# Optimization experiments

Measured on AMD Instinct MI355X. Metric: run time of the kernel, lower is better.

The kernel has to match this reference:

```python
import jax, jax.numpy as jnp
import numpy as np

N = 50000      # nodes
E = 1600000    # edges (avg degree 32)
F_IN = 3       # PROTEINS num_node_features
H = 64         # dim_h
G = 512        # num graphs in batch
C = 2          # PROTEINS num_classes
BN_EPS = 1e-5


def setup_inputs() -> dict:
    key = jax.random.key(0)
    ks = iter(jax.random.split(key, 64))

    def rn(shape, s=0.1):
        return (jax.random.normal(next(ks), shape) * s).astype(jnp.float32)

    inp = {"x": rn((N, F_IN), 1.0)}
    for li, din in ((1, F_IN), (2, H), (3, H)):
        p = f"conv{li}_"
        inp[p + "w1"] = rn((din, H))
        inp[p + "b1"] = rn((H,))
        inp[p + "bn_g"] = jnp.ones((H,), jnp.float32)
        inp[p + "bn_b"] = jnp.zeros((H,), jnp.float32)
        inp[p + "bn_m"] = rn((H,))
        inp[p + "bn_v"] = jax.random.uniform(next(ks), (H,), jnp.float32, 0.5, 1.5)
        inp[p + "w2"] = rn((H, H))
        inp[p + "b2"] = rn((H,))
    inp["lin1_w"] = rn((3 * H, 3 * H))
    inp["lin1_b"] = rn((3 * H,))
    inp["lin2_w"] = rn((3 * H, C))
    inp["lin2_b"] = rn((C,))
    inp["edge_index"] = jax.random.randint(next(ks), (2, E), 0, N, jnp.int64)
    inp["batch"] = jnp.sort(jax.random.randint(next(ks), (N,), 0, G, jnp.int64))
    return inp


def gin_conv(x, src, dst, w1, b1, g, bb, m, v, w2, b2):
    # GINConv, eps=0: mlp(x + sum_{j->i} x_j); aggregate messages at target (dst)
    agg = jax.ops.segment_sum(x[src], dst, num_segments=N)  # [N, d]
    h = x + agg
    h = h @ w1 + b1
    h = (h - m) * jax.lax.rsqrt(v + BN_EPS) * g + bb  # BatchNorm1d (eval)
    h = jax.nn.relu(h)
    h = jax.nn.relu(h @ w2 + b2)
    return h


def reference(x,
              conv1_w1, conv1_b1, conv1_bn_g, conv1_bn_b, conv1_bn_m, conv1_bn_v, conv1_w2, conv1_b2,
              conv2_w1, conv2_b1, conv2_bn_g, conv2_bn_b, conv2_bn_m, conv2_bn_v, conv2_w2, conv2_b2,
              conv3_w1, conv3_b1, conv3_bn_g, conv3_bn_b, conv3_bn_m, conv3_bn_v, conv3_w2, conv3_b2,
              lin1_w, lin1_b, lin2_w, lin2_b,
              edge_index, batch):
    src, dst = edge_index[0], edge_index[1]
    h1 = gin_conv(x,  src, dst, conv1_w1, conv1_b1, conv1_bn_g, conv1_bn_b, conv1_bn_m, conv1_bn_v, conv1_w2, conv1_b2)
    h2 = gin_conv(h1, src, dst, conv2_w1, conv2_b1, conv2_bn_g, conv2_bn_b, conv2_bn_m, conv2_bn_v, conv2_w2, conv2_b2)
    h3 = gin_conv(h2, src, dst, conv3_w1, conv3_b1, conv3_bn_g, conv3_bn_b, conv3_bn_m, conv3_bn_v, conv3_w2, conv3_b2)
    # global_add_pool per graph
    p1 = jax.ops.segment_sum(h1, batch, num_segments=G)
    p2 = jax.ops.segment_sum(h2, batch, num_segments=G)
    p3 = jax.ops.segment_sum(h3, batch, num_segments=G)
    h = jnp.concatenate((p1, p2, p3), axis=1)          # [G, 3H]
    h = jax.nn.relu(h @ lin1_w + lin1_b)
    # dropout p=0.5 is identity in eval mode
    h = h @ lin2_w + lin2_b                            # [G, C]
    return (h, jax.nn.log_softmax(h, axis=1))
```

## Files before the change

### kernel.cpp

```cpp
#include <hip/hip_runtime.h>
#include <hip/hip_bf16.h>
#include <math.h>

#define N_NODES 50000
#define N_EDGES 1600000
#define H 64
#define G_GRAPHS 512
#define C_CLS 2
#define BN_EPS 1e-5f
#define NBUCK 196
#define BUCKCAP 16384
#define E4 (N_EDGES / 4)
#define CSR_BLOCKS ((E4 + 511) / 512)
#define IOP 72

typedef __attribute__((ext_vector_type(8))) short short8;
typedef __attribute__((ext_vector_type(4))) float floatx4;

__device__ __forceinline__ float bflo(unsigned int u) { return __uint_as_float(u << 16); }
__device__ __forceinline__ float bfhi(unsigned int u) { return __uint_as_float(u & 0xffff0000u); }
__device__ __forceinline__ unsigned int bf16_rne(float f) {
    unsigned int u = __float_as_uint(f);
    u += 0x7fffu + ((u >> 16) & 1u);
    return u >> 16;
}

__global__ __launch_bounds__(256) void prep_kernel(
    const float* __restrict__ w2_0, const float* __restrict__ w1_1,
    const float* __restrict__ w2_1, const float* __restrict__ w1_2,
    const float* __restrict__ w2_2, unsigned short* __restrict__ wt,
    const float* __restrict__ x, uint2* __restrict__ xb) {
    int b = blockIdx.x, t = threadIdx.x;
    if (b < 5) {
        const float* w = (b == 0) ? w2_0 : (b == 1) ? w1_1 : (b == 2) ? w2_1
                         : (b == 3) ? w1_2 : w2_2;
        unsigned short* o = wt + b * (H * H);
        for (int idx = t; idx < H * H; idx += 256) {
            int k = idx >> 6, j = idx & 63;
            o[j * H + k] = (unsigned short)bf16_rne(w[idx]);
        }
    } else {
        int node = (b - 5) * 256 + t;
        if (node < N_NODES) {
            uint2 p;
            p.x = bf16_rne(x[node * 3 + 0]) | (bf16_rne(x[node * 3 + 1]) << 16);
            p.y = bf16_rne(x[node * 3 + 2]);
            xb[node] = p;
        }
    }
}

__global__ __launch_bounds__(256) void scatter1_kernel(const int* __restrict__ src,
                                                       const int* __restrict__ dst,
                                                       int* __restrict__ gcnt,
                                                       int* __restrict__ gpacked) {
    __shared__ int bh[NBUCK];
    int t = threadIdx.x;
    if (t < NBUCK) bh[t] = 0;
    __syncthreads();
    int base = blockIdx.x * 512;

    int pkA[4], bkA[4], lrA[4]; bool vA = false;
    int pkB[4], bkB[4], lrB[4]; bool vB = false;
    {
        int i = base + t;
        if (i < E4) {
            vA = true;
            int4 s4 = ((const int4*)src)[i];
            int4 d4 = ((const int4*)dst)[i];
            bkA[0] = d4.x >> 8; pkA[0] = ((d4.x & 255) << 16) | s4.x; lrA[0] = atomicAdd(&bh[bkA[0]], 1);
            bkA[1] = d4.y >> 8; pkA[1] = ((d4.y & 255) << 16) | s4.y; lrA[1] = atomicAdd(&bh[bkA[1]], 1);
            bkA[2] = d4.z >> 8; pkA[2] = ((d4.z & 255) << 16) | s4.z; lrA[2] = atomicAdd(&bh[bkA[2]], 1);
            bkA[3] = d4.w >> 8; pkA[3] = ((d4.w & 255) << 16) | s4.w; lrA[3] = atomicAdd(&bh[bkA[3]], 1);
        }
    }
    {
        int i = base + 256 + t;
        if (i < E4) {
            vB = true;
            int4 s4 = ((const int4*)src)[i];
            int4 d4 = ((const int4*)dst)[i];
            bkB[0] = d4.x >> 8; pkB[0] = ((d4.x & 255) << 16) | s4.x; lrB[0] = atomicAdd(&bh[bkB[0]], 1);
            bkB[1] = d4.y >> 8; pkB[1] = ((d4.y & 255) << 16) | s4.y; lrB[1] = atomicAdd(&bh[bkB[1]], 1);
            bkB[2] = d4.z >> 8; pkB[2] = ((d4.z & 255) << 16) | s4.z; lrB[2] = atomicAdd(&bh[bkB[2]], 1);
            bkB[3] = d4.w >> 8; pkB[3] = ((d4.w & 255) << 16) | s4.w; lrB[3] = atomicAdd(&bh[bkB[3]], 1);
        }
    }
    __syncthreads();
    if (t < NBUCK) {
        int c = bh[t];
        bh[t] = c ? atomicAdd(&gcnt[t], c) : 0;
    }
    __syncthreads();
    if (vA) {
#pragma unroll
        for (int q = 0; q < 4; q++) gpacked[bkA[q] * BUCKCAP + bh[bkA[q]] + lrA[q]] = pkA[q];
    }
    if (vB) {
#pragma unroll
        for (int q = 0; q < 4; q++) gpacked[bkB[q] * BUCKCAP + bh[bkB[q]] + lrB[q]] = pkB[q];
    }
}

__global__ __launch_bounds__(256) void bcsr_kernel(const int* __restrict__ gpacked,
                                                   const int* __restrict__ gcnt,
                                                   int* __restrict__ row_start,
                                                   int* __restrict__ edge_src) {
    __shared__ int cnt[256];
    __shared__ int pref[256];
    int b = blockIdx.x;
    int t = threadIdx.x;

    int v = (t < NBUCK) ? gcnt[t] : 0;
    pref[t] = v;
    __syncthreads();
    for (int off = 1; off < 256; off <<= 1) {
        int u = 0;
        if (t >= off) u = pref[t - off];
        __syncthreads();
        if (t >= off) pref[t] += u;
        __syncthreads();
    }
    int bs = (b > 0) ? pref[b - 1] : 0;
    int cnt_b = gcnt[b];
    if (b == 0 && t == 0) row_start[N_NODES] = N_EDGES;
    __syncthreads();

    const int* gp = gpacked + (size_t)b * BUCKCAP;
    cnt[t] = 0;
    __syncthreads();
    for (int i = t; i < cnt_b; i += 256) atomicAdd(&cnt[gp[i] >> 16], 1);
    __syncthreads();
    int c = cnt[t];
    pref[t] = c;
    __syncthreads();
    for (int off = 1; off < 256; off <<= 1) {
        int u = 0;
        if (t >= off) u = pref[t - off];
        __syncthreads();
        if (t >= off) pref[t] += u;
        __syncthreads();
    }
    int excl = pref[t] - c;
    int node = b * 256 + t;
    if (node < N_NODES) row_start[node] = bs + excl;
    cnt[t] = excl;
    __syncthreads();
    for (int i = t; i < cnt_b; i += 256) {
        int p = gp[i];
        int pos = atomicAdd(&cnt[p >> 16], 1);
        edge_src[bs + pos] = p & 0xffff;
    }
}

__global__ __launch_bounds__(512) void gin1_fused16_kernel(
    const float* __restrict__ x, const uint2* __restrict__ xb,
    const int* __restrict__ row_start, const int* __restrict__ edge_src,
    const float* __restrict__ w1, const float* __restrict__ b1,
    const float* __restrict__ bn_g, const float* __restrict__ bn_b,
    const float* __restrict__ bn_m, const float* __restrict__ bn_v,
    const unsigned short* __restrict__ w2t, const float* __restrict__ b2,
    __hip_bfloat16* __restrict__ hout) {
    __shared__ unsigned short s_mid[16 * IOP];

    int tid = threadIdx.x;
    int wave = tid >> 6, j = tid & 63;
    int nodebase = blockIdx.x * 16;

    float wj0 = w1[j], wj1 = w1[H + j], wj2 = w1[2 * H + j];
    float sc = rsqrtf(bn_v[j] + BN_EPS) * bn_g[j];
    float sh = bn_b[j] - bn_m[j] * sc;
    float bj = b1[j];

    for (int nl = wave * 2; nl < wave * 2 + 2; nl++) {
        int node = nodebase + nl;
        int rs = row_start[node], re = row_start[node + 1];
        float a0 = 0.f, a1 = 0.f, a2 = 0.f;
        for (int t = rs + j; t < re; t += 64) {
            uint2 p = xb[edge_src[t]];
            a0 += bflo(p.x); a1 += bfhi(p.x); a2 += bflo(p.y);
        }
#pragma unroll
        for (int off = 32; off > 0; off >>= 1) {
            a0 += __shfl_xor(a0, off);
            a1 += __shfl_xor(a1, off);
            a2 += __shfl_xor(a2, off);
        }
        float in0 = a0 + x[node * 3 + 0];
        float in1 = a1 + x[node * 3 + 1];
        float in2 = a2 + x[node * 3 + 2];
        float m = bj + in0 * wj0 + in1 * wj1 + in2 * wj2;
        m = fmaxf(m * sc + sh, 0.f);
        s_mid[nl * IOP + j] = (unsigned short)bf16_rne(m);
    }
    __syncthreads();

    if (wave == 0) {
        int quad = j >> 4, l15 = j & 15;
        float bb2[4];
#pragma unroll
        for (int jt = 0; jt < 4; jt++) bb2[jt] = b2[jt * 16 + l15];

        short8 m0 = *(const short8*)&s_mid[l15 * IOP + quad * 8];
        short8 m1 = *(const short8*)&s_mid[l15 * IOP + quad * 8 + 32];
#pragma unroll
        for (int jt = 0; jt < 4; jt++) {
            short8 b0 = *(const short8*)&w2t[(jt * 16 + l15) * H + quad * 8];
            short8 bv = *(const short8*)&w2t[(jt * 16 + l15) * H + quad * 8 + 32];
            floatx4 c = {0.f, 0.f, 0.f, 0.f};
            c = __builtin_amdgcn_mfma_f32_16x16x32_bf16(m0, b0, c, 0, 0, 0);
            c = __builtin_amdgcn_mfma_f32_16x16x32_bf16(m1, bv, c, 0, 0, 0);
#pragma unroll
            for (int r = 0; r < 4; r++) {
                float v = fmaxf(c[r] + bb2[jt], 0.f);
                s_mid[(quad * 4 + r) * IOP + jt * 16 + l15] = (unsigned short)bf16_rne(v);
            }
        }
        unsigned short* ho = (unsigned short*)hout;
#pragma unroll
        for (int cc = 0; cc < 2; cc++) {
            int r = cc * 8 + (j >> 3);
            short8 v = *(const short8*)&s_mid[r * IOP + (j & 7) * 8];
            *(short8*)(ho + (size_t)(nodebase + r) * H + (j & 7) * 8) = v;
        }
    }
}

__global__ __launch_bounds__(512) void gin_fused16_kernel(
    const __hip_bfloat16* __restrict__ hin, const int* __restrict__ row_start,
    const int* __restrict__ edge_src,
    const unsigned short* __restrict__ w1t, const float* __restrict__ b1,
    const float* __restrict__ bn_g, const float* __restrict__ bn_b,
    const float* __restrict__ bn_m, const float* __restrict__ bn_v,
    const unsigned short* __restrict__ w2t, const float* __restrict__ b2,
    __hip_bfloat16* __restrict__ hout) {
    __shared__ unsigned short s_xs[16 * IOP];
    __shared__ unsigned short s_mid[16 * IOP];

    int tid = threadIdx.x;
    int wave = tid >> 6, j = tid & 63;
    int o = j >> 3, jo = j & 7;
    int nodebase = blockIdx.x * 16;

    const char* hb = (const char*)hin;

    for (int nl = wave * 2; nl < wave * 2 + 2; nl++) {
        int node = nodebase + nl;
        int rs = row_start[node], re = row_start[node + 1];
        float a0 = 0.f, a1 = 0.f, a2 = 0.f, a3 = 0.f, a4 = 0.f, a5 = 0.f, a6 = 0.f, a7 = 0.f;
        float b0 = 0.f, b1v = 0.f, b2v = 0.f, b3 = 0.f, b4 = 0.f, b5 = 0.f, b6 = 0.f, b7 = 0.f;
        for (int base = rs; base < re; base += 64) {
            int idx = base + j;
            int sv = (idx < re) ? edge_src[idx] : 0;
            int cnt = min(64, re - base);
            int i = 0;
            for (; i + 16 <= cnt; i += 16) {
                int s0 = __shfl(sv, i + o);
                int s1 = __shfl(sv, i + 8 + o);
                uint4 r0 = *(const uint4*)(hb + (size_t)s0 * 128 + jo * 16);
                uint4 r1 = *(const uint4*)(hb + (size_t)s1 * 128 + jo * 16);
                a0 += bflo(r0.x); a1 += bfhi(r0.x);
                a2 += bflo(r0.y); a3 += bfhi(r0.y);
                a4 += bflo(r0.z); a5 += bfhi(r0.z);
                a6 += bflo(r0.w); a7 += bfhi(r0.w);
                b0 += bflo(r1.x); b1v += bfhi(r1.x);
                b2v += bflo(r1.y); b3 += bfhi(r1.y);
                b4 += bflo(r1.z); b5 += bfhi(r1.z);
                b6 += bflo(r1.w); b7 += bfhi(r1.w);
            }
            for (; i + 8 <= cnt; i += 8) {
                int s = __shfl(sv, i + o);
                uint4 raw = *(const uint4*)(hb + (size_t)s * 128 + jo * 16);
                a0 += bflo(raw.x); a1 += bfhi(raw.x);
                a2 += bflo(raw.y); a3 += bfhi(raw.y);
                a4 += bflo(raw.z); a5 += bfhi(raw.z);
                a6 += bflo(raw.w); a7 += bfhi(raw.w);
            }
            if (i < cnt) {
                int r = cnt - i;
                int s = __shfl(sv, i + (o < r ? o : 0));
                uint4 raw = *(const uint4*)(hb + (size_t)s * 128 + jo * 16);
                if (o < r) {
                    a0 += bflo(raw.x); a1 += bfhi(raw.x);
                    a2 += bflo(raw.y); a3 += bfhi(raw.y);
                    a4 += bflo(raw.z); a5 += bfhi(raw.z);
                    a6 += bflo(raw.w); a7 += bfhi(raw.w);
                }
            }
        }
        a0 += b0; a1 += b1v; a2 += b2v; a3 += b3;
        a4 += b4; a5 += b5; a6 += b6; a7 += b7;
        a0 += __shfl_xor(a0, 8); a0 += __shfl_xor(a0, 16); a0 += __shfl_xor(a0, 32);
        a1 += __shfl_xor(a1, 8); a1 += __shfl_xor(a1, 16); a1 += __shfl_xor(a1, 32);
        a2 += __shfl_xor(a2, 8); a2 += __shfl_xor(a2, 16); a2 += __shfl_xor(a2, 32);
        a3 += __shfl_xor(a3, 8); a3 += __shfl_xor(a3, 16); a3 += __shfl_xor(a3, 32);
        a4 += __shfl_xor(a4, 8); a4 += __shfl_xor(a4, 16); a4 += __shfl_xor(a4, 32);
        a5 += __shfl_xor(a5, 8); a5 += __shfl_xor(a5, 16); a5 += __shfl_xor(a5, 32);
        a6 += __shfl_xor(a6, 8); a6 += __shfl_xor(a6, 16); a6 += __shfl_xor(a6, 32);
        a7 += __shfl_xor(a7, 8); a7 += __shfl_xor(a7, 16); a7 += __shfl_xor(a7, 32);
        if (o == 0) {
            uint4 raw = *(const uint4*)(hb + (size_t)node * 128 + jo * 16);
            a0 += bflo(raw.x); a1 += bfhi(raw.x);
            a2 += bflo(raw.y); a3 += bfhi(raw.y);
            a4 += bflo(raw.z); a5 += bfhi(raw.z);
            a6 += bflo(raw.w); a7 += bfhi(raw.w);
            uint4 ov;
            ov.x = bf16_rne(a0) | (bf16_rne(a1) << 16);
            ov.y = bf16_rne(a2) | (bf16_rne(a3) << 16);
            ov.z = bf16_rne(a4) | (bf16_rne(a5) << 16);
            ov.w = bf16_rne(a6) | (bf16_rne(a7) << 16);
            *(uint4*)&s_xs[nl * IOP + jo * 8] = ov;
        }
    }
    __syncthreads();

    if (wave == 0) {
        int quad = j >> 4, l15 = j & 15;
        float scl[4], sht[4], bb1[4], bb2[4];
#pragma unroll
        for (int jt = 0; jt < 4; jt++) {
            int jj = jt * 16 + l15;
            float sc = rsqrtf(bn_v[jj] + BN_EPS) * bn_g[jj];
            scl[jt] = sc;
            sht[jt] = bn_b[jj] - bn_m[jj] * sc;
            bb1[jt] = b1[jj];
            bb2[jt] = b2[jj];
        }
        short8 a0 = *(const short8*)&s_xs[l15 * IOP + quad * 8];
        short8 a1 = *(const short8*)&s_xs[l15 * IOP + quad * 8 + 32];
#pragma unroll
        for (int jt = 0; jt < 4; jt++) {
            short8 b0 = *(const short8*)&w1t[(jt * 16 + l15) * H + quad * 8];
            short8 bv = *(const short8*)&w1t[(jt * 16 + l15) * H + quad * 8 + 32];
            floatx4 c = {0.f, 0.f, 0.f, 0.f};
            c = __builtin_amdgcn_mfma_f32_16x16x32_bf16(a0, b0, c, 0, 0, 0);
            c = __builtin_amdgcn_mfma_f32_16x16x32_bf16(a1, bv, c, 0, 0, 0);
#pragma unroll
            for (int r = 0; r < 4; r++) {
                float v = (c[r] + bb1[jt]) * scl[jt] + sht[jt];
                v = fmaxf(v, 0.f);
                s_mid[(quad * 4 + r) * IOP + jt * 16 + l15] = (unsigned short)bf16_rne(v);
            }
        }
        short8 m0 = *(const short8*)&s_mid[l15 * IOP + quad * 8];
        short8 m1 = *(const short8*)&s_mid[l15 * IOP + quad * 8 + 32];
#pragma unroll
        for (int jt = 0; jt < 4; jt++) {
            short8 b0 = *(const short8*)&w2t[(jt * 16 + l15) * H + quad * 8];
            short8 bv = *(const short8*)&w2t[(jt * 16 + l15) * H + quad * 8 + 32];
            floatx4 c = {0.f, 0.f, 0.f, 0.f};
            c = __builtin_amdgcn_mfma_f32_16x16x32_bf16(m0, b0, c, 0, 0, 0);
            c = __builtin_amdgcn_mfma_f32_16x16x32_bf16(m1, bv, c, 0, 0, 0);
#pragma unroll
            for (int r = 0; r < 4; r++) {
                float v = fmaxf(c[r] + bb2[jt], 0.f);
                s_xs[(quad * 4 + r) * IOP + jt * 16 + l15] = (unsigned short)bf16_rne(v);
            }
        }
        unsigned short* ho = (unsigned short*)hout;
#pragma unroll
        for (int cc = 0; cc < 2; cc++) {
            int r = cc * 8 + (j >> 3);
            short8 v = *(const short8*)&s_xs[r * IOP + (j & 7) * 8];
            *(short8*)(ho + (size_t)(nodebase + r) * H + (j & 7) * 8) = v;
        }
    }
}

__global__ __launch_bounds__(192) void pool_head_kernel(
    const __hip_bfloat16* __restrict__ h1, const __hip_bfloat16* __restrict__ h2,
    const __hip_bfloat16* __restrict__ h3, const int* __restrict__ batch,
    const float* __restrict__ lin1_w, const float* __restrict__ lin1_b,
    const float* __restrict__ lin2_w, const float* __restrict__ lin2_b,
    float* __restrict__ out) {
    __shared__ float s_row[3 * H];
    __shared__ float s_mid[3 * H];
    __shared__ float s_z[C_CLS];
    __shared__ int s_se[2];

    int g = blockIdx.x;
    int j = threadIdx.x;
    if (j < 2) {
        int target = g + j;
        int lo = 0, hi = N_NODES;
        while (lo < hi) {
            int mid = (lo + hi) >> 1;
            if (batch[mid] < target) lo = mid + 1; else hi = mid;
        }
        s_se[j] = lo;
    }
    __syncthreads();
    int ns = s_se[0], ne = s_se[1];

    int which = j >> 6;
    int f = j & 63;
    const __hip_bfloat16* h = (which == 0) ? h1 : ((which == 1) ? h2 : h3);
    float p0 = 0.f, p1 = 0.f, p2 = 0.f, p3 = 0.f;
    int n = ns;
    for (; n + 3 < ne; n += 4) {
        p0 += __bfloat162float(h[(size_t)n * H + f]);
        p1 += __bfloat162float(h[(size_t)(n + 1) * H + f]);
        p2 += __bfloat162float(h[(size_t)(n + 2) * H + f]);
        p3 += __bfloat162float(h[(size_t)(n + 3) * H + f]);
    }
    for (; n < ne; n++) p0 += __bfloat162float(h[(size_t)n * H + f]);
    s_row[j] = (p0 + p1) + (p2 + p3);
    __syncthreads();

    float acc = lin1_b[j];
    for (int k = 0; k < 3 * H; k++) acc += s_row[k] * lin1_w[k * (3 * H) + j];
    s_mid[j] = fmaxf(acc, 0.f);
    __syncthreads();

    if (j < C_CLS) {
        float z = lin2_b[j];
        for (int k = 0; k < 3 * H; k++) z += s_mid[k] * lin2_w[k * C_CLS + j];
        s_z[j] = z;
    }
    __syncthreads();
    if (j < C_CLS) {
        float z0 = s_z[0], z1 = s_z[1];
        float mx = fmaxf(z0, z1);
        float lse = mx + logf(expf(z0 - mx) + expf(z1 - mx));
        out[g * C_CLS + j] = s_z[j];
        out[G_GRAPHS * C_CLS + g * C_CLS + j] = s_z[j] - lse;
    }
}

extern "C" void kernel_launch(void* const* d_in, const int* in_sizes, int n_in,
                              void* d_out, int out_size, void* d_ws, size_t ws_size,
                              hipStream_t stream) {
    const float* x = (const float*)d_in[0];
    const float* cw1[3], *cb1[3], *cg[3], *cbb[3], *cm[3], *cv[3], *cw2[3], *cb2[3];
    for (int l = 0; l < 3; l++) {
        int b = 1 + 8 * l;
        cw1[l] = (const float*)d_in[b + 0];
        cb1[l] = (const float*)d_in[b + 1];
        cg[l]  = (const float*)d_in[b + 2];
        cbb[l] = (const float*)d_in[b + 3];
        cm[l]  = (const float*)d_in[b + 4];
        cv[l]  = (const float*)d_in[b + 5];
        cw2[l] = (const float*)d_in[b + 6];
        cb2[l] = (const float*)d_in[b + 7];
    }
    const float* lin1_w = (const float*)d_in[25];
    const float* lin1_b = (const float*)d_in[26];
    const float* lin2_w = (const float*)d_in[27];
    const float* lin2_b = (const float*)d_in[28];
    const int* edge_index = (const int*)d_in[29];
    const int* batch = (const int*)d_in[30];
    const int* src = edge_index;
    const int* dst = edge_index + N_EDGES;
    float* out = (float*)d_out;

    int* edge_src = (int*)d_ws;
    int* gpacked = edge_src + N_EDGES;
    int* gcnt = gpacked + (size_t)NBUCK * BUCKCAP;
    int* row_start = gcnt + NBUCK;
    uintptr_t hp = (uintptr_t)(row_start + N_NODES + 2);
    hp = (hp + 127) & ~(uintptr_t)127;
    unsigned short* wt = (unsigned short*)hp;
    uint2* xb = (uint2*)(wt + 5 * H * H);
    __hip_bfloat16* h1 = (__hip_bfloat16*)(xb + N_NODES);
    __hip_bfloat16* h2 = h1 + (size_t)N_NODES * H;
    __hip_bfloat16* h3 = h2 + (size_t)N_NODES * H;

    const unsigned short* w2t_0 = wt + 0 * H * H;
    const unsigned short* w1t_1 = wt + 1 * H * H;
    const unsigned short* w2t_1 = wt + 2 * H * H;
    const unsigned short* w1t_2 = wt + 3 * H * H;
    const unsigned short* w2t_2 = wt + 4 * H * H;

    hipMemsetAsync(gcnt, 0, NBUCK * sizeof(int), stream);
    prep_kernel<<<5 + (N_NODES + 255) / 256, 256, 0, stream>>>(
        cw2[0], cw1[1], cw2[1], cw1[2], cw2[2], wt, x, xb);
    scatter1_kernel<<<CSR_BLOCKS, 256, 0, stream>>>(src, dst, gcnt, gpacked);
    bcsr_kernel<<<NBUCK, 256, 0, stream>>>(gpacked, gcnt, row_start, edge_src);

    const int fgrid = N_NODES / 16;

    gin1_fused16_kernel<<<fgrid, 512, 0, stream>>>(x, xb, row_start, edge_src,
        cw1[0], cb1[0], cg[0], cbb[0], cm[0], cv[0], w2t_0, cb2[0], h1);
    gin_fused16_kernel<<<fgrid, 512, 0, stream>>>(h1, row_start, edge_src,
        w1t_1, cb1[1], cg[1], cbb[1], cm[1], cv[1], w2t_1, cb2[1], h2);
    gin_fused16_kernel<<<fgrid, 512, 0, stream>>>(h2, row_start, edge_src,
        w1t_2, cb1[2], cg[2], cbb[2], cm[2], cv[2], w2t_2, cb2[2], h3);
    pool_head_kernel<<<G_GRAPHS, 3 * H, 0, stream>>>(h1, h2, h3, batch,
        lin1_w, lin1_b, lin2_w, lin2_b, out);
}
```

Before: 281.9 us.

## Fuse global add pooling into GIN layers via atomics and merge per-wave node gathers

Each GIN layer kernel now accumulates its output rows into a per-graph pool buffer with float atomics, using a single atomic when the four MFMA output rows share a graph. This replaces the separate pooling pass that binary-searched the batch array and re-read h1, h2 and h3. Separately, each wave now gathers the edges of its two nodes in one combined loop, splitting them into two accumulator sets by edge position, with wider 4-way unrolled gathers. This removes per-node tail inefficiency for short neighbour lists, at the cost of more registers, branchy accumulation and atomic contention on the pool buffer.

```diff
diff --git a/kernel.cpp b/kernel.cpp
--- a/kernel.cpp
+++ b/kernel.cpp
@@ -153,6 +153,10 @@
     }
 }
 
+#define RED3(A) { A += __shfl_xor(A, 8); A += __shfl_xor(A, 16); A += __shfl_xor(A, 32); }
+#define RED6(A) { A += __shfl_xor(A, 1); A += __shfl_xor(A, 2); A += __shfl_xor(A, 4); \
+                  A += __shfl_xor(A, 8); A += __shfl_xor(A, 16); A += __shfl_xor(A, 32); }
+
 __global__ __launch_bounds__(512) void gin1_fused16_kernel(
     const float* __restrict__ x, const uint2* __restrict__ xb,
     const int* __restrict__ row_start, const int* __restrict__ edge_src,
@@ -160,38 +164,56 @@
     const float* __restrict__ bn_g, const float* __restrict__ bn_b,
     const float* __restrict__ bn_m, const float* __restrict__ bn_v,
     const unsigned short* __restrict__ w2t, const float* __restrict__ b2,
-    __hip_bfloat16* __restrict__ hout) {
+    __hip_bfloat16* __restrict__ hout, const int* __restrict__ batch,
+    float* __restrict__ pool) {
     __shared__ unsigned short s_mid[16 * IOP];
+    __shared__ int s_bat[16];
 
     int tid = threadIdx.x;
     int wave = tid >> 6, j = tid & 63;
     int nodebase = blockIdx.x * 16;
+    if (tid < 16) s_bat[tid] = batch[nodebase + tid];
 
     float wj0 = w1[j], wj1 = w1[H + j], wj2 = w1[2 * H + j];
     float sc = rsqrtf(bn_v[j] + BN_EPS) * bn_g[j];
     float sh = bn_b[j] - bn_m[j] * sc;
     float bj = b1[j];
 
-    for (int nl = wave * 2; nl < wave * 2 + 2; nl++) {
-        int node = nodebase + nl;
-        int rs = row_start[node], re = row_start[node + 1];
-        float a0 = 0.f, a1 = 0.f, a2 = 0.f;
-        for (int t = rs + j; t < re; t += 64) {
-            uint2 p = xb[edge_src[t]];
-            a0 += bflo(p.x); a1 += bfhi(p.x); a2 += bflo(p.y);
-        }
-#pragma unroll
-        for (int off = 32; off > 0; off >>= 1) {
-            a0 += __shfl_xor(a0, off);
-            a1 += __shfl_xor(a1, off);
-            a2 += __shfl_xor(a2, off);
-        }
-        float in0 = a0 + x[node * 3 + 0];
-        float in1 = a1 + x[node * 3 + 1];
-        float in2 = a2 + x[node * 3 + 2];
+    int n0 = nodebase + wave * 2;
+    int rs0 = row_start[n0];
+    int re0 = row_start[n0 + 1];
+    int re1 = row_start[n0 + 2];
+    int c0 = re0 - rs0;
+    int total = re1 - rs0;
+
+    float a00 = 0.f, a01 = 0.f, a02 = 0.f;
+    float a10 = 0.f, a11 = 0.f, a12 = 0.f;
+    for (int base = 0; base < total; base += 64) {
+        int idx = rs0 + base + j;
+        if (idx < re1) {
+            uint2 p = xb[edge_src[idx]];
+            if (base + j < c0) { a00 += bflo(p.x); a01 += bfhi(p.x); a02 += bflo(p.y); }
+            else               { a10 += bflo(p.x); a11 += bfhi(p.x); a12 += bflo(p.y); }
+        }
+    }
+    RED6(a00) RED6(a01) RED6(a02)
+    RED6(a10) RED6(a11) RED6(a12)
+    {
+        float in0 = a00 + x[n0 * 3 + 0];
+        float in1 = a01 + x[n0 * 3 + 1];
+        float in2 = a02 + x[n0 * 3 + 2];
         float m = bj + in0 * wj0 + in1 * wj1 + in2 * wj2;
         m = fmaxf(m * sc + sh, 0.f);
-        s_mid[nl * IOP + j] = (unsigned short)bf16_rne(m);
+        s_mid[(wave * 2) * IOP + j] = (unsigned short)bf16_rne(m);
+    }
+    {
+        int n1 = n0 + 1;
+        float in0 = a10 + x[n1 * 3 + 0];
+        float in1 = a11 + x[n1 * 3 + 1];
+        float in2 = a12 + x[n1 * 3 + 2];
+        float m = bj + in0 * wj0 + in1 * wj1 + in2 * wj2;
+        m = fmaxf(m * sc + sh, 0.f);
+        s_mid[(wave * 2 + 1) * IOP + j] = (unsigned short)bf16_rne(m);
     }
     __syncthreads();
 
@@ -203,6 +225,7 @@
 
         short8 m0 = *(const short8*)&s_mid[l15 * IOP + quad * 8];
         short8 m1 = *(const short8*)&s_mid[l15 * IOP + quad * 8 + 32];
+        int bq0 = s_bat[quad * 4], bq3 = s_bat[quad * 4 + 3];
 #pragma unroll
         for (int jt = 0; jt < 4; jt++) {
             short8 b0 = *(const short8*)&w2t[(jt * 16 + l15) * H + quad * 8];
@@ -210,10 +233,21 @@
             floatx4 c = {0.f, 0.f, 0.f, 0.f};
             c = __builtin_amdgcn_mfma_f32_16x16x32_bf16(m0, b0, c, 0, 0, 0);
             c = __builtin_amdgcn_mfma_f32_16x16x32_bf16(m1, bv, c, 0, 0, 0);
+            float vv[4];
 #pragma unroll
             for (int r = 0; r < 4; r++) {
                 float v = fmaxf(c[r] + bb2[jt], 0.f);
+                vv[r] = v;
                 s_mid[(quad * 4 + r) * IOP + jt * 16 + l15] = (unsigned short)bf16_rne(v);
+            }
+            int jj = jt * 16 + l15;
+            if (bq0 == bq3) {
+                atomicAdd(&pool[bq0 * 192 + jj], (vv[0] + vv[1]) + (vv[2] + vv[3]));
+            } else {
+                atomicAdd(&pool[s_bat[quad * 4 + 0] * 192 + jj], vv[0]);
+                atomicAdd(&pool[s_bat[quad * 4 + 1] * 192 + jj], vv[1]);
+                atomicAdd(&pool[s_bat[quad * 4 + 2] * 192 + jj], vv[2]);
+                atomicAdd(&pool[s_bat[quad * 4 + 3] * 192 + jj], vv[3]);
             }
         }
         unsigned short* ho = (unsigned short*)hout;
@@ -225,6 +259,16 @@
         }
     }
 }
+
+#define ACC8(R, A0, A1, A2, A3, A4, A5, A6, A7) { \
+    A0 += bflo(R.x); A1 += bfhi(R.x); A2 += bflo(R.y); A3 += bfhi(R.y); \
+    A4 += bflo(R.z); A5 += bfhi(R.z); A6 += bflo(R.w); A7 += bfhi(R.w); }
+
+#define GROUP_ACC(R, r) { \
+    if ((r) < lim) { \
+        if ((base + (r)) < c0) { ACC8(R, a00, a01, a02, a03, a04, a05, a06, a07) } \
+        else                   { ACC8(R, a10, a11, a12, a13, a14, a15, a16, a17) } \
+    } }
 
 __global__ __launch_bounds__(512) void gin_fused16_kernel(
     const __hip_bfloat16* __restrict__ hin, const int* __restrict__ row_start,
@@ -233,84 +277,72 @@
     const float* __restrict__ bn_g, const float* __restrict__ bn_b,
     const float* __restrict__ bn_m, const float* __restrict__ bn_v,
     const unsigned short* __restrict__ w2t, const float* __restrict__ b2,
-    __hip_bfloat16* __restrict__ hout) {
+    __hip_bfloat16* __restrict__ hout, const int* __restrict__ batch,
+    float* __restrict__ pool) {
     __shared__ unsigned short s_xs[16 * IOP];
     __shared__ unsigned short s_mid[16 * IOP];
+    __shared__ int s_bat[16];
 
     int tid = threadIdx.x;
     int wave = tid >> 6, j = tid & 63;
     int o = j >> 3, jo = j & 7;
     int nodebase = blockIdx.x * 16;
+    if (tid < 16) s_bat[tid] = batch[nodebase + tid];
 
     const char* hb = (const char*)hin;
 
-    for (int nl = wave * 2; nl < wave * 2 + 2; nl++) {
-        int node = nodebase + nl;
-        int rs = row_start[node], re = row_start[node + 1];
-        float a0 = 0.f, a1 = 0.f, a2 = 0.f, a3 = 0.f, a4 = 0.f, a5 = 0.f, a6 = 0.f, a7 = 0.f;
-        float b0 = 0.f, b1v = 0.f, b2v = 0.f, b3 = 0.f, b4 = 0.f, b5 = 0.f, b6 = 0.f, b7 = 0.f;
-        for (int base = rs; base < re; base += 64) {
-            int idx = base + j;
-            int sv = (idx < re) ? edge_src[idx] : 0;
-            int cnt = min(64, re - base);
-            int i = 0;
-            for (; i + 16 <= cnt; i += 16) {
-                int s0 = __shfl(sv, i + o);
-                int s1 = __shfl(sv, i + 8 + o);
-                uint4 r0 = *(const uint4*)(hb + (size_t)s0 * 128 + jo * 16);
-                uint4 r1 = *(const uint4*)(hb + (size_t)s1 * 128 + jo * 16);
-                a0 += bflo(r0.x); a1 += bfhi(r0.x);
-                a2 += bflo(r0.y); a3 += bfhi(r0.y);
-                a4 += bflo(r0.z); a5 += bfhi(r0.z);
-                a6 += bflo(r0.w); a7 += bfhi(r0.w);
-                b0 += bflo(r1.x); b1v += bfhi(r1.x);
-                b2v += bflo(r1.y); b3 += bfhi(r1.y);
-                b4 += bflo(r1.z); b5 += bfhi(r1.z);
-                b6 += bflo(r1.w); b7 += bfhi(r1.w);
-            }
-            for (; i + 8 <= cnt; i += 8) {
-                int s = __shfl(sv, i + o);
-                uint4 raw = *(const uint4*)(hb + (size_t)s * 128 + jo * 16);
-                a0 += bflo(raw.x); a1 += bfhi(raw.x);
-                a2 += bflo(raw.y); a3 += bfhi(raw.y);
-                a4 += bflo(raw.z); a5 += bfhi(raw.z);
-                a6 += bflo(raw.w); a7 += bfhi(raw.w);
-            }
-            if (i < cnt) {
-                int r = cnt - i;
-                int s = __shfl(sv, i + (o < r ? o : 0));
-                uint4 raw = *(const uint4*)(hb + (size_t)s * 128 + jo * 16);
-                if (o < r) {
-                    a0 += bflo(raw.x); a1 += bfhi(raw.x);
-                    a2 += bflo(raw.y); a3 += bfhi(raw.y);
-                    a4 += bflo(raw.z); a5 += bfhi(raw.z);
-                    a6 += bflo(raw.w); a7 += bfhi(raw.w);
-                }
-            }
-        }
-        a0 += b0; a1 += b1v; a2 += b2v; a3 += b3;
-        a4 += b4; a5 += b5; a6 += b6; a7 += b7;
-        a0 += __shfl_xor(a0, 8); a0 += __shfl_xor(a0, 16); a0 += __shfl_xor(a0, 32);
-        a1 += __shfl_xor(a1, 8); a1 += __shfl_xor(a1, 16); a1 += __shfl_xor(a1, 32);
-        a2 += __shfl_xor(a2, 8); a2 += __shfl_xor(a2, 16); a2 += __shfl_xor(a2, 32);
-        a3 += __shfl_xor(a3, 8); a3 += __shfl_xor(a3, 16); a3 += __shfl_xor(a3, 32);
-        a4 += __shfl_xor(a4, 8); a4 += __shfl_xor(a4, 16); a4 += __shfl_xor(a4, 32);
-        a5 += __shfl_xor(a5, 8); a5 += __shfl_xor(a5, 16); a5 += __shfl_xor(a5, 32);
-        a6 += __shfl_xor(a6, 8); a6 += __shfl_xor(a6, 16); a6 += __shfl_xor(a6, 32);
-        a7 += __shfl_xor(a7, 8); a7 += __shfl_xor(a7, 16); a7 += __shfl_xor(a7, 32);
-        if (o == 0) {
-            uint4 raw = *(const uint4*)(hb + (size_t)node * 128 + jo * 16);
-            a0 += bflo(raw.x); a1 += bfhi(raw.x);
-            a2 += bflo(raw.y); a3 += bfhi(raw.y);
-            a4 += bflo(raw.z); a5 += bfhi(raw.z);
-            a6 += bflo(raw.w); a7 += bfhi(raw.w);
-            uint4 ov;
-            ov.x = bf16_rne(a0) | (bf16_rne(a1) << 16);
-            ov.y = bf16_rne(a2) | (bf16_rne(a3) << 16);
-            ov.z = bf16_rne(a4) | (bf16_rne(a5) << 16);
-            ov.w = bf16_rne(a6) | (bf16_rne(a7) << 16);
-            *(uint4*)&s_xs[nl * IOP + jo * 8] = ov;
-        }
+    int n0 = nodebase + wave * 2;
+    int rs0 = row_start[n0];
+    int re0 = row_start[n0 + 1];
+    int re1 = row_start[n0 + 2];
+    int c0 = re0 - rs0;
+    int total = re1 - rs0;
+
+    float a00 = 0.f, a01 = 0.f, a02 = 0.f, a03 = 0.f, a04 = 0.f, a05 = 0.f, a06 = 0.f, a07 = 0.f;
+    float a10 = 0.f, a11 = 0.f, a12 = 0.f, a13 = 0.f, a14 = 0.f, a15 = 0.f, a16 = 0.f, a17 = 0.f;
+
+    for (int base = 0; base < total; base += 64) {
+        int idx = rs0 + base + j;
+        int sv = (idx < re1) ? edge_src[idx] : 0;
+        int lim = min(64, total - base);
+#pragma unroll
+        for (int i = 0; i < 64; i += 32) {
+            if (i >= lim) break;
+            int r0 = i + o, r1 = i + 8 + o, r2 = i + 16 + o, r3 = i + 24 + o;
+            int s0 = __shfl(sv, r0);
+            int s1 = __shfl(sv, r1);
+            int s2 = __shfl(sv, r2);
+            int s3 = __shfl(sv, r3);
+            uint4 R0 = *(const uint4*)(hb + (size_t)s0 * 128 + jo * 16);
+            uint4 R1 = *(const uint4*)(hb + (size_t)s1 * 128 + jo * 16);
+            uint4 R2 = *(const uint4*)(hb + (size_t)s2 * 128 + jo * 16);
+            uint4 R3 = *(const uint4*)(hb + (size_t)s3 * 128 + jo * 16);
+            GROUP_ACC(R0, r0)
+            GROUP_ACC(R1, r1)
+            GROUP_ACC(R2, r2)
+            GROUP_ACC(R3, r3)
+        }
+    }
+    RED3(a00) RED3(a01) RED3(a02) RED3(a03) RED3(a04) RED3(a05) RED3(a06) RED3(a07)
+    RED3(a10) RED3(a11) RED3(a12) RED3(a13) RED3(a14) RED3(a15) RED3(a16) RED3(a17)
+
+    if (o < 2) {
+        int nl = wave * 2 + o;
+        float r0 = (o == 0) ? a00 : a10, r1 = (o == 0) ? a01 : a11;
+        float r2 = (o == 0) ? a02 : a12, r3 = (o == 0) ? a03 : a13;
+        float r4 = (o == 0) ? a04 : a14, r5 = (o == 0) ? a05 : a15;
+        float r6 = (o == 0) ? a06 : a16, r7 = (o == 0) ? a07 : a17;
+        uint4 raw = *(const uint4*)(hb + (size_t)(nodebase + nl) * 128 + jo * 16);
+        r0 += bflo(raw.x); r1 += bfhi(raw.x);
+        r2 += bflo(raw.y); r3 += bfhi(raw.y);
+        r4 += bflo(raw.z); r5 += bfhi(raw.z);
+        r6 += bflo(raw.w); r7 += bfhi(raw.w);
+        uint4 ov;
+        ov.x = bf16_rne(r0) | (bf16_rne(r1) << 16);
+        ov.y = bf16_rne(r2) | (bf16_rne(r3) << 16);
+        ov.z = bf16_rne(r4) | (bf16_rne(r5) << 16);
+        ov.w = bf16_rne(r6) | (bf16_rne(r7) << 16);
+        *(uint4*)&s_xs[nl * IOP + jo * 8] = ov;
     }
     __syncthreads();
 
@@ -344,6 +376,7 @@
         }
         short8 m0 = *(const short8*)&s_mid[l15 * IOP + quad * 8];
         short8 m1 = *(const short8*)&s_mid[l15 * IOP + quad * 8 + 32];
+        int bq0 = s_bat[quad * 4], bq3 = s_bat[quad * 4 + 3];
 #pragma unroll
         for (int jt = 0; jt < 4; jt++) {
             short8 b0 = *(const short8*)&w2t[(jt * 16 + l15) * H + quad * 8];
@@ -351,10 +384,21 @@
             floatx4 c = {0.f, 0.f, 0.f, 0.f};
             c = __builtin_amdgcn_mfma_f32_16x16x32_bf16(m0, b0, c, 0, 0, 0);
             c = __builtin_amdgcn_mfma_f32_16x16x32_bf16(m1, bv, c, 0, 0, 0);
+            float vv[4];
 #pragma unroll
             for (int r = 0; r < 4; r++) {
                 float v = fmaxf(c[r] + bb2[jt], 0.f);
+                vv[r] = v;
                 s_xs[(quad * 4 + r) * IOP + jt * 16 + l15] = (unsigned short)bf16_rne(v);
+            }
+            int jj = jt * 16 + l15;
+            if (bq0 == bq3) {
+                atomicAdd(&pool[bq0 * 192 + jj], (vv[0] + vv[1]) + (vv[2] + vv[3]));
+            } else {
+                atomicAdd(&pool[s_bat[quad * 4 + 0] * 192 + jj], vv[0]);
+                atomicAdd(&pool[s_bat[quad * 4 + 1] * 192 + jj], vv[1]);
+                atomicAdd(&pool[s_bat[quad * 4 + 2] * 192 + jj], vv[2]);
+                atomicAdd(&pool[s_bat[quad * 4 + 3] * 192 + jj], vv[3]);
             }
         }
         unsigned short* ho = (unsigned short*)hout;
@@ -367,44 +411,18 @@
     }
 }
 
-__global__ __launch_bounds__(192) void pool_head_kernel(
-    const __hip_bfloat16* __restrict__ h1, const __hip_bfloat16* __restrict__ h2,
-    const __hip_bfloat16* __restrict__ h3, const int* __restrict__ batch,
+__global__ __launch_bounds__(192) void head_kernel(
+    const float* __restrict__ pool,
     const float* __restrict__ lin1_w, const float* __restrict__ lin1_b,
     const float* __restrict__ lin2_w, const float* __restrict__ lin2_b,
     float* __restrict__ out) {
     __shared__ float s_row[3 * H];
     __shared__ float s_mid[3 * H];
     __shared__ float s_z[C_CLS];
-    __shared__ int s_se[2];
 
     int g = blockIdx.x;
     int j = threadIdx.x;
-    if (j < 2) {
-        int target = g + j;
-        int lo = 0, hi = N_NODES;
-        while (lo < hi) {
-            int mid = (lo + hi) >> 1;
-            if (batch[mid] < target) lo = mid + 1; else hi = mid;
-        }
-        s_se[j] = lo;
-    }
-    __syncthreads();
-    int ns = s_se[0], ne = s_se[1];
-
-    int which = j >> 6;
-    int f = j & 63;
-    const __hip_bfloat16* h = (which == 0) ? h1 : ((which == 1) ? h2 : h3);
-    float p0 = 0.f, p1 = 0.f, p2 = 0.f, p3 = 0.f;
-    int n = ns;
-    for (; n + 3 < ne; n += 4) {
-        p0 += __bfloat162float(h[(size_t)n * H + f]);
-        p1 += __bfloat162float(h[(size_t)(n + 1) * H + f]);
-        p2 += __bfloat162float(h[(size_t)(n + 2) * H + f]);
-        p3 += __bfloat162float(h[(size_t)(n + 3) * H + f]);
-    }
-    for (; n < ne; n++) p0 += __bfloat162float(h[(size_t)n * H + f]);
-    s_row[j] = (p0 + p1) + (p2 + p3);
+    s_row[j] = pool[g * 192 + j];
     __syncthreads();
 
     float acc = lin1_b[j];
@@ -456,7 +474,8 @@
     int* edge_src = (int*)d_ws;
     int* gpacked = edge_src + N_EDGES;
     int* gcnt = gpacked + (size_t)NBUCK * BUCKCAP;
-    int* row_start = gcnt + NBUCK;
+    float* pool = (float*)(gcnt + NBUCK);
+    int* row_start = (int*)(pool + G_GRAPHS * 3 * H);
     uintptr_t hp = (uintptr_t)(row_start + N_NODES + 2);
     hp = (hp + 127) & ~(uintptr_t)127;
     unsigned short* wt = (unsigned short*)hp;
@@ -471,7 +490,7 @@
     const unsigned short* w1t_2 = wt + 3 * H * H;
     const unsigned short* w2t_2 = wt + 4 * H * H;
 
-    hipMemsetAsync(gcnt, 0, NBUCK * sizeof(int), stream);
+    hipMemsetAsync(gcnt, 0, NBUCK * sizeof(int) + G_GRAPHS * 3 * H * sizeof(float), stream);
     prep_kernel<<<5 + (N_NODES + 255) / 256, 256, 0, stream>>>(
         cw2[0], cw1[1], cw2[1], cw1[2], cw2[2], wt, x, xb);
     scatter1_kernel<<<CSR_BLOCKS, 256, 0, stream>>>(src, dst, gcnt, gpacked);
@@ -480,11 +499,11 @@
     const int fgrid = N_NODES / 16;
 
     gin1_fused16_kernel<<<fgrid, 512, 0, stream>>>(x, xb, row_start, edge_src,
-        cw1[0], cb1[0], cg[0], cbb[0], cm[0], cv[0], w2t_0, cb2[0], h1);
+        cw1[0], cb1[0], cg[0], cbb[0], cm[0], cv[0], w2t_0, cb2[0], h1, batch, pool);
     gin_fused16_kernel<<<fgrid, 512, 0, stream>>>(h1, row_start, edge_src,
-        w1t_1, cb1[1], cg[1], cbb[1], cm[1], cv[1], w2t_1, cb2[1], h2);
+        w1t_1, cb1[1], cg[1], cbb[1], cm[1], cv[1], w2t_1, cb2[1], h2, batch, pool + 64);
     gin_fused16_kernel<<<fgrid, 512, 0, stream>>>(h2, row_start, edge_src,
-        w1t_2, cb1[2], cg[2], cbb[2], cm[2], cv[2], w2t_2, cb2[2], h3);
-    pool_head_kernel<<<G_GRAPHS, 3 * H, 0, stream>>>(h1, h2, h3, batch,
+        w1t_2, cb1[2], cg[2], cbb[2], cm[2], cv[2], w2t_2, cb2[2], h3, batch, pool + 128);
+    head_kernel<<<G_GRAPHS, 3 * H, 0, stream>>>(pool,
         lin1_w, lin1_b, lin2_w, lin2_b, out);
 }
```

After: 289.4 us. +2.6%, slower.
